# Kernel tuning notes

Measured on AMD Instinct MI355X. Metric: run time of the kernel, lower is better.

Reference implementation:

```python
import jax, jax.numpy as jnp
import numpy as np

L, B, H, S, D = 28, 3, 16, 1024, 128
VOCAB = 151936
HIST = 64
BEAM_SIZE = 3
TOP_K = 3


def setup_inputs() -> dict:
    key = jax.random.key(0)
    k1, k2, k3, k4 = jax.random.split(key, 4)
    kv = jax.random.normal(k1, (L, B, H, S, D), dtype=jnp.float32)
    logits = jax.random.normal(k2, (B, VOCAB), dtype=jnp.float32)
    save_id = jax.random.randint(k3, (B, HIST), 0, VOCAB, dtype=jnp.int32)
    repeat_penality = jnp.ones((B, VOCAB), dtype=jnp.float32)
    previous_prob = jax.random.normal(k4, (B, 1), dtype=jnp.float32)
    penality_value = jnp.ones((1,), dtype=jnp.float32)
    return {
        "kv": kv,
        "logits": logits,
        "save_id": save_id,
        "repeat_penality": repeat_penality,
        "previous_prob": previous_prob,
        "penality_value": penality_value,
        "beam_size": BEAM_SIZE,
        "topK": TOP_K,
    }


def reference(kv, logits, save_id, repeat_penality, previous_prob, penality_value, beam_size, topK):
    # log_softmax over penalized logits  [beam, vocab]
    lp = jax.nn.log_softmax(logits * repeat_penality, axis=-1)
    # per-beam top-k (sorted, largest)  [beam, topK]
    top_k_prob, top_k_idx = jax.lax.top_k(lp, topK)
    # combine with running beam log-probs and flatten  [beam*topK]
    current_prob = (top_k_prob + previous_prob).reshape(-1)
    # global top-beam selection over beam*topK candidates
    top_beam_prob, top_beam_idx = jax.lax.top_k(current_prob, beam_size)
    beam_index = top_beam_idx // topK                       # [beam] source beam per survivor
    tokens = top_k_idx.reshape(-1)[top_beam_idx]            # [beam] chosen token ids
    # reorder all per-layer KV caches by surviving beams (the heavy gather)
    kv_out = kv[:, beam_index]                              # [L, beam, H, S, D]
    # reorder + update repeat penalty at chosen tokens
    rp = repeat_penality[beam_index]                        # [beam, vocab]
    rp = rp.at[jnp.arange(beam_size), tokens].multiply(penality_value[0])
    tok_col = tokens[:, None].astype(jnp.int32)             # [beam, 1]
    save_id_out = jnp.concatenate([save_id[beam_index], tok_col], axis=-1)
    max_logits_idx = tok_col[0]                             # [1]
    return (kv_out, tok_col, save_id_out, rp, top_beam_prob[:, None], max_logits_idx)
```

## Files before the change

kernel.cpp:

```cpp
#include <hip/hip_runtime.h>
#include <math.h>

#define NL 28
#define NB 3
#define NH 16
#define NS 1024
#define ND 128
#define VOCAB 151936
#define HIST 64

#define CHUNKS 64
#define CHUNK_LEN (VOCAB / CHUNKS)

#define OFF_TOK  176160768
#define OFF_SAVE 176160771
#define OFF_RP   176160966
#define OFF_PROB 176616774
#define OFF_MAX  176616777

#define WS_BEAM 1536
#define WS_TOK  1540

typedef float f32x4 __attribute__((ext_vector_type(4)));

__device__ __forceinline__ void ins3(float x, int ix, float v[3], int iv[3]) {
    if (x > v[0] || (x == v[0] && ix < iv[0])) {
        v[2] = v[1]; iv[2] = iv[1];
        v[1] = v[0]; iv[1] = iv[0];
        v[0] = x;    iv[0] = ix;
    } else if (x > v[1] || (x == v[1] && ix < iv[1])) {
        v[2] = v[1]; iv[2] = iv[1];
        v[1] = x;    iv[1] = ix;
    } else if (x > v[2] || (x == v[2] && ix < iv[2])) {
        v[2] = x;    iv[2] = ix;
    }
}

__global__ __launch_bounds__(256) void k1_partial(
    const float* __restrict__ logits, const float* __restrict__ rpen,
    float* __restrict__ wsf, int* __restrict__ wsi) {
    const int b = blockIdx.x / CHUNKS;
    const int c = blockIdx.x % CHUNKS;
    const int base = c * CHUNK_LEN;
    const float* lrow = logits + b * VOCAB;
    const float* prow = rpen + b * VOCAB;

    float m = -INFINITY, l = 0.f;
    float v[3] = {-INFINITY, -INFINITY, -INFINITY};
    int iv[3] = {-1, -1, -1};

    for (int j = threadIdx.x; j < CHUNK_LEN; j += 256) {
        int idx = base + j;
        float x = lrow[idx] * prow[idx];
        if (x > m) { l = l * expf(m - x) + 1.f; m = x; }
        else       { l += expf(x - m); }
        ins3(x, idx, v, iv);
    }

    for (int off = 32; off > 0; off >>= 1) {
        float om = __shfl_down(m, off, 64);
        float ol = __shfl_down(l, off, 64);
        float ov[3]; int oi[3];
#pragma unroll
        for (int k = 0; k < 3; ++k) {
            ov[k] = __shfl_down(v[k], off, 64);
            oi[k] = __shfl_down(iv[k], off, 64);
        }
        float M = fmaxf(m, om);
        l = l * expf(m - M) + ol * expf(om - M);
        m = M;
#pragma unroll
        for (int k = 0; k < 3; ++k) ins3(ov[k], oi[k], v, iv);
    }

    __shared__ float sm[4], sl[4], sv[4][3];
    __shared__ int si[4][3];
    const int lane = threadIdx.x & 63;
    const int wid = threadIdx.x >> 6;
    if (lane == 0) {
        sm[wid] = m; sl[wid] = l;
#pragma unroll
        for (int k = 0; k < 3; ++k) { sv[wid][k] = v[k]; si[wid][k] = iv[k]; }
    }
    __syncthreads();
    if (threadIdx.x == 0) {
        for (int w = 1; w < 4; ++w) {
            float M = fmaxf(m, sm[w]);
            l = l * expf(m - M) + sl[w] * expf(sm[w] - M);
            m = M;
#pragma unroll
            for (int k = 0; k < 3; ++k) ins3(sv[w][k], si[w][k], v, iv);
        }
        const int pbase = (b * CHUNKS + c) * 8;
        wsf[pbase + 0] = m;
        wsf[pbase + 1] = l;
#pragma unroll
        for (int k = 0; k < 3; ++k) {
            wsf[pbase + 2 + k] = v[k];
            wsi[pbase + 5 + k] = iv[k];
        }
    }
}

__global__ __launch_bounds__(256) void k2_select(
    const float* __restrict__ prev, const int* __restrict__ save_id,
    const float* __restrict__ wsf, int* __restrict__ wsi,
    float* __restrict__ out) {
    __shared__ float stopv[9];
    __shared__ int stopi[9];
    __shared__ int sbeam[3], stok[3];
    __shared__ float sprob[3];
    const int t = threadIdx.x;

    if (t < NB) {
        float m = -INFINITY, l = 0.f;
        float v[3] = {-INFINITY, -INFINITY, -INFINITY};
        int iv[3] = {-1, -1, -1};
        for (int c = 0; c < CHUNKS; ++c) {
            const int pbase = (t * CHUNKS + c) * 8;
            float pm = wsf[pbase + 0], pl = wsf[pbase + 1];
            float M = fmaxf(m, pm);
            l = l * expf(m - M) + pl * expf(pm - M);
            m = M;
#pragma unroll
            for (int k = 0; k < 3; ++k) ins3(wsf[pbase + 2 + k], wsi[pbase + 5 + k], v, iv);
        }
        const float lse = m + logf(l);
#pragma unroll
        for (int k = 0; k < 3; ++k) {
            stopv[t * 3 + k] = v[k] - lse;
            stopi[t * 3 + k] = iv[k];
        }
    }
    __syncthreads();
    if (t == 0) {
        float cur[9];
        for (int j = 0; j < 9; ++j) cur[j] = stopv[j] + prev[j / 3];
        bool used[9] = {false, false, false, false, false, false, false, false, false};
        for (int i = 0; i < 3; ++i) {
            int best = 0; float bv = -INFINITY;
            for (int j = 0; j < 9; ++j) {
                if (!used[j] && cur[j] > bv) { bv = cur[j]; best = j; }
            }
            used[best] = true;
            sbeam[i] = best / 3;
            stok[i]  = stopi[best];
            sprob[i] = bv;
        }
        for (int i = 0; i < 3; ++i) {
            wsi[WS_BEAM + i] = sbeam[i];
            wsi[WS_TOK + i]  = stok[i];
        }
    }
    __syncthreads();
    if (t < 3) {
        out[OFF_TOK + t]  = (float)stok[t];
        out[OFF_PROB + t] = sprob[t];
    }
    if (t == 0) out[OFF_MAX] = (float)stok[0];
    if (t < 3 * (HIST + 1)) {
        const int i = t / (HIST + 1);
        const int h = t - i * (HIST + 1);
        out[OFF_SAVE + t] = (h < HIST) ? (float)save_id[sbeam[i] * HIST + h]
                                       : (float)stok[i];
    }
}

#define PER4      ((NH * NS * ND) / 4)
#define KV4       (NL * NB * PER4)
#define KVBLOCKS  (KV4 / 2048)
#define RPBLOCKS  ((NB * VOCAB + 255) / 256)

__global__ __launch_bounds__(256) void k3_fused(
    const f32x4* __restrict__ kv, const float* __restrict__ rpen,
    const float* __restrict__ pen, const int* __restrict__ wsi,
    f32x4* __restrict__ out4, float* __restrict__ out) {
    if (blockIdx.x < KVBLOCKS) {
        const unsigned li = blockIdx.x >> 8;
        const unsigned l  = li / 3u;
        const unsigned i  = li - l * 3u;
        const int sb = wsi[WS_BEAM + i];
        const unsigned dst = blockIdx.x * 2048u + threadIdx.x;
        const unsigned src = (l * 3u + (unsigned)sb) * PER4
                           + (blockIdx.x & 255u) * 2048u + threadIdx.x;
        f32x4 r[8];
#pragma unroll
        for (int k = 0; k < 8; ++k)
            r[k] = __builtin_nontemporal_load(&kv[src + k * 256u]);
#pragma unroll
        for (int k = 0; k < 8; ++k)
            __builtin_nontemporal_store(r[k], &out4[dst + k * 256u]);
    } else {
        const int idx = (blockIdx.x - KVBLOCKS) * 256 + threadIdx.x;
        if (idx < NB * VOCAB) {
            const int i = idx / VOCAB;
            const int v = idx - i * VOCAB;
            float x = rpen[wsi[WS_BEAM + i] * VOCAB + v];
            if (v == wsi[WS_TOK + i]) x *= pen[0];
            out[OFF_RP + idx] = x;
        }
    }
}

extern "C" void kernel_launch(void* const* d_in, const int* in_sizes, int n_in,
                              void* d_out, int out_size, void* d_ws, size_t ws_size,
                              hipStream_t stream) {
    const float* kv      = (const float*)d_in[0];
    const float* logits  = (const float*)d_in[1];
    const int*   save_id = (const int*)d_in[2];
    const float* rpen    = (const float*)d_in[3];
    const float* prev    = (const float*)d_in[4];
    const float* pen     = (const float*)d_in[5];
    float* out = (float*)d_out;
    float* wsf = (float*)d_ws;
    int*   wsi = (int*)d_ws;

    k1_partial<<<NB * CHUNKS, 256, 0, stream>>>(logits, rpen, wsf, wsi);
    k2_select<<<1, 256, 0, stream>>>(prev, save_id, wsf, wsi, out);
    k3_fused<<<KVBLOCKS + RPBLOCKS, 256, 0, stream>>>(
        (const f32x4*)kv, rpen, pen, wsi, (f32x4*)out, out);
}
```

Baseline: 1.112 ms.

## Restructure KV gather as persistent grid looping over slabs with shared beam map

The KV gather kernel now launches a fixed grid of 2048 blocks instead of one block per 2048-vector chunk. Each thread copies one f32x4 position from every layer/beam slab, four slabs per iteration, using a slab-to-source map built in shared memory. The repeat-penalty reorder is folded into the same threads rather than handled by extra blocks. Nontemporal loads and stores are replaced by plain loads and stores, which changes cache behaviour, and each thread keeps only four loads in flight instead of eight.

```diff
diff --git a/kernel.cpp b/kernel.cpp
--- a/kernel.cpp
+++ b/kernel.cpp
@@ -167,38 +167,52 @@
 }
 
 #define PER4      ((NH * NS * ND) / 4)
-#define KV4       (NL * NB * PER4)
-#define KVBLOCKS  (KV4 / 2048)
-#define RPBLOCKS  ((NB * VOCAB + 255) / 256)
+#define NSLAB     (NL * NB)
+#define KVBLOCKS  2048
 
 __global__ __launch_bounds__(256) void k3_fused(
     const f32x4* __restrict__ kv, const float* __restrict__ rpen,
     const float* __restrict__ pen, const int* __restrict__ wsi,
     f32x4* __restrict__ out4, float* __restrict__ out) {
-    if (blockIdx.x < KVBLOCKS) {
-        const unsigned li = blockIdx.x >> 8;
-        const unsigned l  = li / 3u;
-        const unsigned i  = li - l * 3u;
-        const int sb = wsi[WS_BEAM + i];
-        const unsigned dst = blockIdx.x * 2048u + threadIdx.x;
-        const unsigned src = (l * 3u + (unsigned)sb) * PER4
-                           + (blockIdx.x & 255u) * 2048u + threadIdx.x;
-        f32x4 r[8];
-#pragma unroll
-        for (int k = 0; k < 8; ++k)
-            r[k] = __builtin_nontemporal_load(&kv[src + k * 256u]);
-#pragma unroll
-        for (int k = 0; k < 8; ++k)
-            __builtin_nontemporal_store(r[k], &out4[dst + k * 256u]);
-    } else {
-        const int idx = (blockIdx.x - KVBLOCKS) * 256 + threadIdx.x;
-        if (idx < NB * VOCAB) {
-            const int i = idx / VOCAB;
-            const int v = idx - i * VOCAB;
-            float x = rpen[wsi[WS_BEAM + i] * VOCAB + v];
-            if (v == wsi[WS_TOK + i]) x *= pen[0];
-            out[OFF_RP + idx] = x;
-        }
+    __shared__ int smap[NSLAB];
+    __shared__ int sbeam[3], stok[3];
+    const int t = threadIdx.x;
+    if (t < 3) {
+        sbeam[t] = wsi[WS_BEAM + t];
+        stok[t]  = wsi[WS_TOK + t];
+    }
+    __syncthreads();
+    if (t < NSLAB) {
+        const int l = t / 3;
+        const int i = t - l * 3;
+        smap[t] = l * 3 + sbeam[i];
+    }
+    __syncthreads();
+
+    const unsigned p = blockIdx.x * 256u + (unsigned)t;
+
+#pragma unroll 1
+    for (int k = 0; k < NSLAB; k += 4) {
+        const size_t s0 = (size_t)smap[k + 0] * PER4 + p;
+        const size_t s1 = (size_t)smap[k + 1] * PER4 + p;
+        const size_t s2 = (size_t)smap[k + 2] * PER4 + p;
+        const size_t s3 = (size_t)smap[k + 3] * PER4 + p;
+        f32x4 r0 = kv[s0];
+        f32x4 r1 = kv[s1];
+        f32x4 r2 = kv[s2];
+        f32x4 r3 = kv[s3];
+        out4[(size_t)(k + 0) * PER4 + p] = r0;
+        out4[(size_t)(k + 1) * PER4 + p] = r1;
+        out4[(size_t)(k + 2) * PER4 + p] = r2;
+        out4[(size_t)(k + 3) * PER4 + p] = r3;
+    }
+
+    if (p < NB * VOCAB) {
+        const int i = p / VOCAB;
+        const int v = (int)p - i * VOCAB;
+        float x = rpen[sbeam[i] * VOCAB + v];
+        if (v == stok[i]) x *= pen[0];
+        out[OFF_RP + p] = x;
     }
 }
 
@@ -217,6 +231,6 @@
 
     k1_partial<<<NB * CHUNKS, 256, 0, stream>>>(logits, rpen, wsf, wsi);
     k2_select<<<1, 256, 0, stream>>>(prev, save_id, wsf, wsi, out);
-    k3_fused<<<KVBLOCKS + RPBLOCKS, 256, 0, stream>>>(
+    k3_fused<<<KVBLOCKS, 256, 0, stream>>>(
         (const f32x4*)kv, rpen, pen, wsi, (f32x4*)out, out);
 }
```

Result: no change. 1.110 ms (-0.1%).
